# Kernel optimization log

Measured on AMD Instinct MI355X. Metric: run time of the kernel, lower is better.

Reference implementation:

```python
import jax, jax.numpy as jnp
import numpy as np

D = 512   # feature_dim
H = 256   # hidden_dim


def setup_inputs() -> dict:
    key = jax.random.key(0)
    ks = jax.random.split(key, 7)
    s = 1.0 / np.sqrt(H)
    return {
        "x": jax.random.normal(ks[0], (128, 512, D), dtype=jnp.float32),
        "W_ih": jax.random.uniform(ks[1], (4 * H, D), jnp.float32, -s, s),
        "W_hh": jax.random.uniform(ks[2], (4 * H, H), jnp.float32, -s, s),
        "b_ih": jax.random.uniform(ks[3], (4 * H,), jnp.float32, -s, s),
        "b_hh": jax.random.uniform(ks[4], (4 * H,), jnp.float32, -s, s),
        "fc_w": jax.random.uniform(ks[5], (1, H), jnp.float32, -s, s),
        "fc_b": jax.random.uniform(ks[6], (1,), jnp.float32, -s, s),
    }


def _lstm_last_hidden(x, W_ih, W_hh, b_ih, b_hh):
    # x: [B, S, D]. PyTorch gate order: i, f, g, o.
    B = x.shape[0]
    # Precompute input projections for all timesteps: [S, B, 4H]
    xg = jnp.einsum('bsd,gd->sbg', x, W_ih) + (b_ih + b_hh)

    def step(carry, xg_t):
        h, c = carry
        gates = xg_t + h @ W_hh.T  # [B, 4H]
        i, f, g, o = jnp.split(gates, 4, axis=-1)
        c = jax.nn.sigmoid(f) * c + jax.nn.sigmoid(i) * jnp.tanh(g)
        h = jax.nn.sigmoid(o) * jnp.tanh(c)
        return (h, c), None

    h0 = jnp.zeros((B, H), x.dtype)
    c0 = jnp.zeros((B, H), x.dtype)
    (h_n, _), _ = jax.lax.scan(step, (h0, c0), xg)
    return h_n  # [B, H]


def reference(x, W_ih, W_hh, b_ih, b_hh, fc_w, fc_b):
    h_n = _lstm_last_hidden(x, W_ih, W_hh, b_ih, b_hh)
    logits = h_n @ fc_w.T + fc_b  # [B, 1]
    return logits
```

## Files before the change

kernel.cpp:

```cpp
#include <hip/hip_runtime.h>
#include <stdint.h>

typedef _Float16 f16;
typedef _Float16 f16x2 __attribute__((ext_vector_type(2)));
typedef _Float16 f16x8 __attribute__((ext_vector_type(8)));
typedef float f32x4 __attribute__((ext_vector_type(4)));

#define SEQ   512
#define BATCH 128
#define DIM   512
#define HID   256
#define G4    1024

typedef const __attribute__((address_space(1))) void* gas1p;
typedef __attribute__((address_space(3))) void* las3p;

__device__ __forceinline__ uint32_t pk2(float a, float b){
  return __builtin_bit_cast(uint32_t, __builtin_amdgcn_cvt_pkrtz(a, b));
}

__device__ __forceinline__ int sdot4(uint32_t a, uint32_t b, int c){
#if __has_builtin(__builtin_amdgcn_sdot4)
  return __builtin_amdgcn_sdot4(a, b, c, false);
#else
  int s = c;
  #pragma unroll
  for (int i = 0; i < 4; ++i){
    int ai = (int)(signed char)((a >> (8*i)) & 0xff);
    int bi = (int)(signed char)((b >> (8*i)) & 0xff);
    s += ai*bi;
  }
  return s;
#endif
}

__device__ __forceinline__ float sigm(float x){
  return __builtin_amdgcn_rcpf(1.0f + __expf(-x));
}
__device__ __forceinline__ float tanh_(float x){
  return 1.0f - 2.0f*__builtin_amdgcn_rcpf(__expf(2.0f*x) + 1.0f);
}

__global__ void __launch_bounds__(256) cvt_f16_kernel(const float* __restrict__ in,
                                                      f16* __restrict__ out, int n8){
  int i = blockIdx.x*blockDim.x + threadIdx.x;
  if (i >= n8) return;
  const float4* p = (const float4*)in;
  float4 a = p[2*i], b = p[2*i+1];
  uint4 r;
  r.x = pk2(a.x, a.y); r.y = pk2(a.z, a.w);
  r.z = pk2(b.x, b.y); r.w = pk2(b.z, b.w);
  ((uint4*)out)[i] = r;
}

__global__ void __launch_bounds__(256) prep_whh8(const float* __restrict__ Whh,
                                                 uint32_t* __restrict__ W8L){
  int p = blockIdx.x*256 + threadIdx.x;
  int t  = p >> 7;
  int r  = (p >> 5) & 3;
  int qq = p & 31;
  int lane  = t & 63;
  int j     = (t >> 6)*32 + (lane & 31);
  int khalf = (lane >> 5) & 1;
  int g  = j + (r << 8);
  int kw = khalf*32 + qq;
  float4 v = *(const float4*)(Whh + g*HID + kw*4);
  int a = __float2int_rn(v.x*2048.f); a = a > 127 ? 127 : (a < -127 ? -127 : a);
  int b = __float2int_rn(v.y*2048.f); b = b > 127 ? 127 : (b < -127 ? -127 : b);
  int c = __float2int_rn(v.z*2048.f); c = c > 127 ? 127 : (c < -127 ? -127 : c);
  int d = __float2int_rn(v.w*2048.f); d = d > 127 ? 127 : (d < -127 ? -127 : d);
  W8L[p] = (uint32_t)(a & 0xff) | ((uint32_t)(b & 0xff) << 8) |
           ((uint32_t)(c & 0xff) << 16) | ((uint32_t)(d & 0xff) << 24);
}

#define BM 128
#define BN 128
#define BK 64

__global__ void __launch_bounds__(256) gemm_xg_kernel(const f16* __restrict__ A,
                                                      const f16* __restrict__ Bm,
                                                      const float* __restrict__ bih,
                                                      const float* __restrict__ bhh,
                                                      f16* __restrict__ C){
  __shared__ __align__(16) f16 ldsA[BM*BK];
  __shared__ __align__(16) f16 ldsB[BN*BK];
  const int tid  = threadIdx.x;
  const int wave = tid >> 6;
  const int lane = tid & 63;
  const int bid  = blockIdx.x;
  const int nt   = bid & 7;
  const int mt   = bid >> 3;
  const long m0  = (long)mt * BM;
  const int n0   = nt * BN;
  const int wm   = wave >> 1, wn = wave & 1;
  const int lrow = lane >> 3;
  const int lk   = (lane & 7) * 8;

  f32x4 acc[4][4];
  #pragma unroll
  for (int i=0;i<4;++i)
    #pragma unroll
    for (int j=0;j<4;++j) acc[i][j] = (f32x4){0.f,0.f,0.f,0.f};

  auto ldsAq = (__attribute__((address_space(3))) char*)ldsA;
  auto ldsBq = (__attribute__((address_space(3))) char*)ldsB;

  for (int kt = 0; kt < DIM/BK; ++kt){
    const int k0 = kt*BK;
    __syncthreads();
    #pragma unroll
    for (int i = 0; i < 4; ++i){
      const int seg = wave*4 + i;
      const f16* ga = A  + (m0 + seg*8 + lrow)*DIM + (k0 + lk);
      const f16* gb = Bm + (long)(n0 + seg*8 + lrow)*DIM + (k0 + lk);
      __builtin_amdgcn_global_load_lds((gas1p)ga, (las3p)(ldsAq + seg*1024), 16, 0, 0);
      __builtin_amdgcn_global_load_lds((gas1p)gb, (las3p)(ldsBq + seg*1024), 16, 0, 0);
    }
    __syncthreads();
    #pragma unroll
    for (int kk = 0; kk < 2; ++kk){
      f16x8 af[4], bf[4];
      const int kb = kk*32 + (lane>>4)*8;
      #pragma unroll
      for (int mi=0; mi<4; ++mi){
        af[mi] = *(const f16x8*)(ldsA + (wm*64 + mi*16 + (lane&15))*BK + kb);
        bf[mi] = *(const f16x8*)(ldsB + (wn*64 + mi*16 + (lane&15))*BK + kb);
      }
      #pragma unroll
      for (int mi=0;mi<4;++mi)
        #pragma unroll
        for (int ni=0;ni<4;++ni)
          acc[mi][ni] = __builtin_amdgcn_mfma_f32_16x16x32_f16(af[mi], bf[ni], acc[mi][ni], 0,0,0);
    }
  }
  float bias[4];
  #pragma unroll
  for (int ni=0;ni<4;++ni){
    int col = n0 + wn*64 + ni*16 + (lane&15);
    bias[ni] = bih[col] + bhh[col];
  }
  #pragma unroll
  for (int mi=0;mi<4;++mi){
    #pragma unroll
    for (int ni=0;ni<4;++ni){
      int col = n0 + wn*64 + ni*16 + (lane&15);
      int cpos = (col & 255)*4 + (col >> 8);
      #pragma unroll
      for (int r=0;r<4;++r){
        long row = m0 + wm*64 + mi*16 + (lane>>4)*4 + r;
        C[row*G4 + cpos] = (f16)(acc[mi][ni][r] + bias[ni]);
      }
    }
  }
}

__global__ void
__attribute__((amdgpu_flat_work_group_size(512, 512), amdgpu_waves_per_eu(2, 2)))
lstm8_kernel(const f16* __restrict__ xq,
             const uint32_t* __restrict__ W8L,
             const float* __restrict__ fcw,
             const float* __restrict__ fcb,
             float* __restrict__ out){
  __shared__ __align__(16) uint8_t h8[2][256];
  __shared__ float red[256];
  const int t = threadIdx.x;
  const int b = blockIdx.x;
  const int lane  = t & 63;
  const int j     = (t >> 6)*32 + (lane & 31);
  const int khalf = lane >> 5;
  const float invS = 1.0f / (2048.0f * 127.0f);

  uint32_t w[128];
  {
    const uint4* wp = (const uint4*)(W8L + (size_t)t*128);
    #pragma unroll
    for (int q8 = 0; q8 < 32; ++q8){
      uint4 u = wp[q8];
      w[4*q8+0] = u.x; w[4*q8+1] = u.y; w[4*q8+2] = u.z; w[4*q8+3] = u.w;
    }
  }
  #pragma unroll
  for (int i = 0; i < 128; ++i) asm volatile("" : "+v"(w[i]));

  if (t < 128) ((uint32_t*)h8)[t] = 0;

  const f16* xrow = xq + (long)b * SEQ * G4;
  ushort4 xv = *(const ushort4*)(xrow + j*4);
  float c = 0.f, hlast = 0.f;
  __syncthreads();

  for (int ts = 0; ts < SEQ; ++ts){
    ushort4 xc = xv;
    if (ts + 1 < SEQ) xv = *(const ushort4*)(xrow + (ts+1)*G4 + j*4);

    const uint4* hq = (const uint4*)&h8[ts & 1][khalf*128];
    uint4 hv[8];
    #pragma unroll
    for (int q = 0; q < 8; ++q) hv[q] = hq[q];

    int acc[4] = {0, 0, 0, 0};
    #pragma unroll
    for (int q = 0; q < 8; ++q){
      #pragma unroll
      for (int r = 0; r < 4; ++r){
        acc[r] = sdot4(w[r*32+4*q+0], hv[q].x, acc[r]);
        acc[r] = sdot4(w[r*32+4*q+1], hv[q].y, acc[r]);
        acc[r] = sdot4(w[r*32+4*q+2], hv[q].z, acc[r]);
        acc[r] = sdot4(w[r*32+4*q+3], hv[q].w, acc[r]);
      }
    }
    #pragma unroll
    for (int r = 0; r < 4; ++r) acc[r] += __shfl_xor(acc[r], 32);

    f16 xi  = __builtin_bit_cast(f16, xc.x), xf = __builtin_bit_cast(f16, xc.y);
    f16 xg_ = __builtin_bit_cast(f16, xc.z), xo = __builtin_bit_cast(f16, xc.w);
    float gi = (float)xi  + (float)acc[0]*invS;
    float gf = (float)xf  + (float)acc[1]*invS;
    float gg = (float)xg_ + (float)acc[2]*invS;
    float go = (float)xo  + (float)acc[3]*invS;
    float iv = sigm(gi), fv = sigm(gf), gv = tanh_(gg), ov = sigm(go);
    c     = fv*c + iv*gv;
    hlast = ov * tanh_(c);
    int hq8 = __float2int_rn(hlast * 127.f);
    if (khalf == 0) h8[(ts+1) & 1][j] = (uint8_t)(hq8 & 0xff);
    __syncthreads();
  }

  if (khalf == 0) red[j] = hlast * fcw[j];
  __syncthreads();
  if (t < 64){
    float s = red[t] + red[t+64] + red[t+128] + red[t+192];
    #pragma unroll
    for (int off = 32; off; off >>= 1) s += __shfl_down(s, off);
    if (t == 0) out[b] = s + fcb[0];
  }
}

extern "C" void kernel_launch(void* const* d_in, const int* in_sizes, int n_in,
                              void* d_out, int out_size, void* d_ws, size_t ws_size,
                              hipStream_t stream) {
  const float* x   = (const float*)d_in[0];
  const float* Wih = (const float*)d_in[1];
  const float* Whh = (const float*)d_in[2];
  const float* bih = (const float*)d_in[3];
  const float* bhh = (const float*)d_in[4];
  const float* fcw = (const float*)d_in[5];
  const float* fcb = (const float*)d_in[6];
  float* out = (float*)d_out;

  char* ws = (char*)d_ws;
  f16*      xh  = (f16*)ws;
  f16*      Wh  = (f16*)(ws + 67108864);
  f16*      xq  = (f16*)(ws + 68157440);
  uint32_t* W8L = (uint32_t*)(ws + 202375168);

  cvt_f16_kernel<<<16384, 256, 0, stream>>>(x,   xh, 33554432/8);
  cvt_f16_kernel<<<256,   256, 0, stream>>>(Wih, Wh, 524288/8);
  prep_whh8<<<256, 256, 0, stream>>>(Whh, W8L);
  gemm_xg_kernel<<<4096, 256, 0, stream>>>(xh, Wh, bih, bhh, xq);
  lstm8_kernel<<<BATCH, 512, 0, stream>>>(xq, W8L, fcw, fcb, out);
}
```

Baseline: 661.7 us.

## Use one thread per hidden unit in LSTM recurrence, o-gate weights in LDS

The recurrent kernel drops from 512 threads, with two threads per hidden unit splitting K and combining through a cross-lane shuffle, to 256 threads that each compute the full 256-long dot product for one hidden unit. The i, f and g gate weights (192 words) stay in registers, and the o-gate weights move to 64KB of dynamic LDS, read every step. The prep kernel writes the weights in these two new layouts. This removes the shuffle and halves the thread count, but doubles the serial dot-product chain per thread and adds LDS reads each timestep.

```diff
diff --git a/kernel.cpp b/kernel.cpp
--- a/kernel.cpp
+++ b/kernel.cpp
@@ -39,6 +39,11 @@
 }
 __device__ __forceinline__ float tanh_(float x){
   return 1.0f - 2.0f*__builtin_amdgcn_rcpf(__expf(2.0f*x) + 1.0f);
+}
+
+__device__ __forceinline__ int q8(float v){
+  int a = __float2int_rn(v * 2048.f);
+  return a > 127 ? 127 : (a < -127 ? -127 : a);
 }
 
 __global__ void __launch_bounds__(256) cvt_f16_kernel(const float* __restrict__ in,
@@ -54,23 +59,29 @@
 }
 
 __global__ void __launch_bounds__(256) prep_whh8(const float* __restrict__ Whh,
-                                                 uint32_t* __restrict__ W8L){
+                                                 uint32_t* __restrict__ W8R,
+                                                 uint32_t* __restrict__ W8O){
   int p = blockIdx.x*256 + threadIdx.x;
-  int t  = p >> 7;
-  int r  = (p >> 5) & 3;
-  int qq = p & 31;
-  int lane  = t & 63;
-  int j     = (t >> 6)*32 + (lane & 31);
-  int khalf = (lane >> 5) & 1;
-  int g  = j + (r << 8);
-  int kw = khalf*32 + qq;
+  int g, kw;
+  uint32_t* dst;
+  int idx;
+  if (p < 49152){
+    int t = p / 192, rem = p % 192;
+    int r = rem >> 6;
+    kw = rem & 63;
+    g = t + (r << 8);
+    dst = W8R; idx = p;
+  } else {
+    int pB = p - 49152;
+    int q4 = pB >> 10, t = (pB >> 2) & 255, w = pB & 3;
+    kw = q4*4 + w;
+    g = t + 768;
+    dst = W8O; idx = pB;
+  }
   float4 v = *(const float4*)(Whh + g*HID + kw*4);
-  int a = __float2int_rn(v.x*2048.f); a = a > 127 ? 127 : (a < -127 ? -127 : a);
-  int b = __float2int_rn(v.y*2048.f); b = b > 127 ? 127 : (b < -127 ? -127 : b);
-  int c = __float2int_rn(v.z*2048.f); c = c > 127 ? 127 : (c < -127 ? -127 : c);
-  int d = __float2int_rn(v.w*2048.f); d = d > 127 ? 127 : (d < -127 ? -127 : d);
-  W8L[p] = (uint32_t)(a & 0xff) | ((uint32_t)(b & 0xff) << 8) |
-           ((uint32_t)(c & 0xff) << 16) | ((uint32_t)(d & 0xff) << 24);
+  int a = q8(v.x), b = q8(v.y), c = q8(v.z), d = q8(v.w);
+  dst[idx] = (uint32_t)(a & 0xff) | ((uint32_t)(b & 0xff) << 8) |
+             ((uint32_t)(c & 0xff) << 16) | ((uint32_t)(d & 0xff) << 24);
 }
 
 #define BM 128
@@ -155,78 +166,73 @@
 }
 
 __global__ void
-__attribute__((amdgpu_flat_work_group_size(512, 512), amdgpu_waves_per_eu(2, 2)))
+__attribute__((amdgpu_flat_work_group_size(256, 256), amdgpu_waves_per_eu(1, 1)))
 lstm8_kernel(const f16* __restrict__ xq,
-             const uint32_t* __restrict__ W8L,
+             const uint32_t* __restrict__ W8R,
+             const uint4* __restrict__ W8O,
              const float* __restrict__ fcw,
              const float* __restrict__ fcb,
              float* __restrict__ out){
-  __shared__ __align__(16) uint8_t h8[2][256];
-  __shared__ float red[256];
+  extern __shared__ __align__(16) char smem[];
+  uint4*   WoL = (uint4*)smem;
+  uint8_t* h8  = (uint8_t*)(smem + 65536);
+  float*   red = (float*)(smem + 66048);
   const int t = threadIdx.x;
   const int b = blockIdx.x;
-  const int lane  = t & 63;
-  const int j     = (t >> 6)*32 + (lane & 31);
-  const int khalf = lane >> 5;
   const float invS = 1.0f / (2048.0f * 127.0f);
 
-  uint32_t w[128];
+  #pragma unroll
+  for (int i = 0; i < 16; ++i) WoL[i*256 + t] = W8O[i*256 + t];
+
+  uint4 w4[48];
   {
-    const uint4* wp = (const uint4*)(W8L + (size_t)t*128);
-    #pragma unroll
-    for (int q8 = 0; q8 < 32; ++q8){
-      uint4 u = wp[q8];
-      w[4*q8+0] = u.x; w[4*q8+1] = u.y; w[4*q8+2] = u.z; w[4*q8+3] = u.w;
-    }
-  }
-  #pragma unroll
-  for (int i = 0; i < 128; ++i) asm volatile("" : "+v"(w[i]));
+    const uint4* wp = (const uint4*)(W8R + (size_t)t*192);
+    #pragma unroll
+    for (int i = 0; i < 48; ++i) w4[i] = wp[i];
+  }
 
   if (t < 128) ((uint32_t*)h8)[t] = 0;
-
   const f16* xrow = xq + (long)b * SEQ * G4;
-  ushort4 xv = *(const ushort4*)(xrow + j*4);
+  ushort4 xv = *(const ushort4*)(xrow + t*4);
   float c = 0.f, hlast = 0.f;
   __syncthreads();
 
   for (int ts = 0; ts < SEQ; ++ts){
     ushort4 xc = xv;
-    if (ts + 1 < SEQ) xv = *(const ushort4*)(xrow + (ts+1)*G4 + j*4);
-
-    const uint4* hq = (const uint4*)&h8[ts & 1][khalf*128];
-    uint4 hv[8];
-    #pragma unroll
-    for (int q = 0; q < 8; ++q) hv[q] = hq[q];
-
-    int acc[4] = {0, 0, 0, 0};
-    #pragma unroll
-    for (int q = 0; q < 8; ++q){
-      #pragma unroll
-      for (int r = 0; r < 4; ++r){
-        acc[r] = sdot4(w[r*32+4*q+0], hv[q].x, acc[r]);
-        acc[r] = sdot4(w[r*32+4*q+1], hv[q].y, acc[r]);
-        acc[r] = sdot4(w[r*32+4*q+2], hv[q].z, acc[r]);
-        acc[r] = sdot4(w[r*32+4*q+3], hv[q].w, acc[r]);
-      }
-    }
-    #pragma unroll
-    for (int r = 0; r < 4; ++r) acc[r] += __shfl_xor(acc[r], 32);
+    if (ts + 1 < SEQ) xv = *(const ushort4*)(xrow + (ts+1)*G4 + t*4);
+
+    const uint4* hq = (const uint4*)&h8[(ts & 1)*256];
+    int a0 = 0, a1 = 0, a2 = 0, a3 = 0;
+    #pragma unroll
+    for (int q4 = 0; q4 < 16; ++q4){
+      uint4 hv = hq[q4];
+      uint4 wo = WoL[q4*256 + t];
+      uint4 wi = w4[q4], wf = w4[16 + q4], wg = w4[32 + q4];
+      a0 = sdot4(wi.x, hv.x, a0); a0 = sdot4(wi.y, hv.y, a0);
+      a0 = sdot4(wi.z, hv.z, a0); a0 = sdot4(wi.w, hv.w, a0);
+      a1 = sdot4(wf.x, hv.x, a1); a1 = sdot4(wf.y, hv.y, a1);
+      a1 = sdot4(wf.z, hv.z, a1); a1 = sdot4(wf.w, hv.w, a1);
+      a2 = sdot4(wg.x, hv.x, a2); a2 = sdot4(wg.y, hv.y, a2);
+      a2 = sdot4(wg.z, hv.z, a2); a2 = sdot4(wg.w, hv.w, a2);
+      a3 = sdot4(wo.x, hv.x, a3); a3 = sdot4(wo.y, hv.y, a3);
+      a3 = sdot4(wo.z, hv.z, a3); a3 = sdot4(wo.w, hv.w, a3);
+    }
 
     f16 xi  = __builtin_bit_cast(f16, xc.x), xf = __builtin_bit_cast(f16, xc.y);
     f16 xg_ = __builtin_bit_cast(f16, xc.z), xo = __builtin_bit_cast(f16, xc.w);
-    float gi = (float)xi  + (float)acc[0]*invS;
-    float gf = (float)xf  + (float)acc[1]*invS;
-    float gg = (float)xg_ + (float)acc[2]*invS;
-    float go = (float)xo  + (float)acc[3]*invS;
+    float gi = (float)xi  + (float)a0*invS;
+    float gf = (float)xf  + (float)a1*invS;
+    float gg = (float)xg_ + (float)a2*invS;
+    float go = (float)xo  + (float)a3*invS;
     float iv = sigm(gi), fv = sigm(gf), gv = tanh_(gg), ov = sigm(go);
     c     = fv*c + iv*gv;
     hlast = ov * tanh_(c);
-    int hq8 = __float2int_rn(hlast * 127.f);
-    if (khalf == 0) h8[(ts+1) & 1][j] = (uint8_t)(hq8 & 0xff);
+    int hv8 = __float2int_rn(hlast * 127.f);
+    h8[((ts+1) & 1)*256 + t] = (uint8_t)(hv8 & 0xff);
     __syncthreads();
   }
 
-  if (khalf == 0) red[j] = hlast * fcw[j];
+  red[t] = hlast * fcw[t];
   __syncthreads();
   if (t < 64){
     float s = red[t] + red[t+64] + red[t+128] + red[t+192];
@@ -252,11 +258,15 @@
   f16*      xh  = (f16*)ws;
   f16*      Wh  = (f16*)(ws + 67108864);
   f16*      xq  = (f16*)(ws + 68157440);
-  uint32_t* W8L = (uint32_t*)(ws + 202375168);
+  uint32_t* W8R = (uint32_t*)(ws + 202375168);
+  uint32_t* W8O = (uint32_t*)(ws + 202571776);
 
   cvt_f16_kernel<<<16384, 256, 0, stream>>>(x,   xh, 33554432/8);
   cvt_f16_kernel<<<256,   256, 0, stream>>>(Wih, Wh, 524288/8);
-  prep_whh8<<<256, 256, 0, stream>>>(Whh, W8L);
+  prep_whh8<<<256, 256, 0, stream>>>(Whh, W8R, W8O);
   gemm_xg_kernel<<<4096, 256, 0, stream>>>(xh, Wh, bih, bhh, xq);
-  lstm8_kernel<<<BATCH, 512, 0, stream>>>(xq, W8L, fcw, fcb, out);
-}
+  (void)hipFuncSetAttribute(reinterpret_cast<const void*>(lstm8_kernel),
+                            hipFuncAttributeMaxDynamicSharedMemorySize, 67072);
+  lstm8_kernel<<<BATCH, 256, 67072, stream>>>(xq, W8R, (const uint4*)W8O,
+                                              fcw, fcb, out);
+}
```

After: 671.5 us. No clear change (+1.5%).

## Split int8 W_hh across LDS, global/L2 and registers in LSTM recurrence

Applied to the files above, without the earlier changes.

The W_hh int8 weights are no longer held entirely in 128 VGPRs per thread. They are split three ways: 6 of 16 column chunks live in LDS (96KB of dynamic shared memory), 6 are streamed from global memory through L2 each step, and 4 stay in registers. The work is also remapped so each thread computes two gates over the full K dimension instead of four gates over half of K. This removes the per-gate cross-half shuffle and replaces it with a single shuffle that exchanges i*g. The intent is to free registers and raise occupancy or ILP, at the cost of LDS and L2 traffic on every serial timestep.

```diff
diff --git a/kernel.cpp b/kernel.cpp
--- a/kernel.cpp
+++ b/kernel.cpp
@@ -34,11 +34,28 @@
 #endif
 }
 
+__device__ __forceinline__ int dotq(uint4 w, uint4 h, int acc){
+  acc = sdot4(w.x, h.x, acc);
+  acc = sdot4(w.y, h.y, acc);
+  acc = sdot4(w.z, h.z, acc);
+  acc = sdot4(w.w, h.w, acc);
+  return acc;
+}
+
 __device__ __forceinline__ float sigm(float x){
   return __builtin_amdgcn_rcpf(1.0f + __expf(-x));
 }
 __device__ __forceinline__ float tanh_(float x){
   return 1.0f - 2.0f*__builtin_amdgcn_rcpf(__expf(2.0f*x) + 1.0f);
+}
+
+__device__ __forceinline__ uint32_t q8pack(float4 v){
+  int a = __float2int_rn(v.x*2048.f); a = a > 127 ? 127 : (a < -127 ? -127 : a);
+  int b = __float2int_rn(v.y*2048.f); b = b > 127 ? 127 : (b < -127 ? -127 : b);
+  int c = __float2int_rn(v.z*2048.f); c = c > 127 ? 127 : (c < -127 ? -127 : c);
+  int d = __float2int_rn(v.w*2048.f); d = d > 127 ? 127 : (d < -127 ? -127 : d);
+  return (uint32_t)(a & 0xff) | ((uint32_t)(b & 0xff) << 8) |
+         ((uint32_t)(c & 0xff) << 16) | ((uint32_t)(d & 0xff) << 24);
 }
 
 __global__ void __launch_bounds__(256) cvt_f16_kernel(const float* __restrict__ in,
@@ -54,23 +71,35 @@
 }
 
 __global__ void __launch_bounds__(256) prep_whh8(const float* __restrict__ Whh,
-                                                 uint32_t* __restrict__ W8L){
-  int p = blockIdx.x*256 + threadIdx.x;
-  int t  = p >> 7;
-  int r  = (p >> 5) & 3;
-  int qq = p & 31;
-  int lane  = t & 63;
-  int j     = (t >> 6)*32 + (lane & 31);
-  int khalf = (lane >> 5) & 1;
-  int g  = j + (r << 8);
-  int kw = khalf*32 + qq;
-  float4 v = *(const float4*)(Whh + g*HID + kw*4);
-  int a = __float2int_rn(v.x*2048.f); a = a > 127 ? 127 : (a < -127 ? -127 : a);
-  int b = __float2int_rn(v.y*2048.f); b = b > 127 ? 127 : (b < -127 ? -127 : b);
-  int c = __float2int_rn(v.z*2048.f); c = c > 127 ? 127 : (c < -127 ? -127 : c);
-  int d = __float2int_rn(v.w*2048.f); d = d > 127 ? 127 : (d < -127 ? -127 : d);
-  W8L[p] = (uint32_t)(a & 0xff) | ((uint32_t)(b & 0xff) << 8) |
-           ((uint32_t)(c & 0xff) << 16) | ((uint32_t)(d & 0xff) << 24);
+                                                 uint4* __restrict__ WL,
+                                                 uint4* __restrict__ WG,
+                                                 uint4* __restrict__ WR){
+  int tid = blockIdx.x*256 + threadIdx.x;
+  int r, Q; uint4* dst; int idx;
+  if (tid < 6144){
+    const int QLt[6] = {0,1,2,8,9,10};
+    int q = tid >> 10; r = tid & 1023;
+    Q = QLt[q]; dst = WL; idx = tid;
+  } else if (tid < 12288){
+    const int QGt[6] = {3,4,5,11,12,13};
+    int i = tid - 6144;
+    int q = i >> 10; r = i & 1023;
+    Q = QGt[q]; dst = WG; idx = i;
+  } else {
+    const int QRt[4] = {6,7,14,15};
+    int i = tid - 12288;
+    int t = i >> 3, s = i & 7;
+    int lane = t & 63, wave = t >> 6;
+    int j = wave*32 + (lane & 31), p = lane >> 5;
+    r = (s < 4) ? (j + p*256) : (j + p*256 + 512);
+    Q = QRt[s & 3]; dst = WR; idx = i;
+  }
+  const float* src = Whh + r*HID + Q*16;
+  float4 v0 = *(const float4*)(src);
+  float4 v1 = *(const float4*)(src + 4);
+  float4 v2 = *(const float4*)(src + 8);
+  float4 v3 = *(const float4*)(src + 12);
+  dst[idx] = make_uint4(q8pack(v0), q8pack(v1), q8pack(v2), q8pack(v3));
 }
 
 #define BM 128
@@ -155,78 +184,118 @@
 }
 
 __global__ void
-__attribute__((amdgpu_flat_work_group_size(512, 512), amdgpu_waves_per_eu(2, 2)))
+__attribute__((amdgpu_flat_work_group_size(512, 512)))
 lstm8_kernel(const f16* __restrict__ xq,
-             const uint32_t* __restrict__ W8L,
+             const uint4* __restrict__ WLg,
+             const uint4* __restrict__ WG,
+             const uint4* __restrict__ WR,
              const float* __restrict__ fcw,
              const float* __restrict__ fcb,
              float* __restrict__ out){
-  __shared__ __align__(16) uint8_t h8[2][256];
-  __shared__ float red[256];
+  extern __shared__ __align__(16) char smem[];
+  uint4*   WL  = (uint4*)smem;
+  uint8_t* h8  = (uint8_t*)(smem + 98304);
+  float*   red = (float*)(smem + 98816);
   const int t = threadIdx.x;
   const int b = blockIdx.x;
-  const int lane  = t & 63;
-  const int j     = (t >> 6)*32 + (lane & 31);
-  const int khalf = lane >> 5;
+  const int lane = t & 63, wave = t >> 6;
+  const int j = wave*32 + (lane & 31);
+  const int p = lane >> 5;
   const float invS = 1.0f / (2048.0f * 127.0f);
 
-  uint32_t w[128];
+  #pragma unroll
+  for (int i = 0; i < 12; ++i) WL[i*512 + t] = WLg[i*512 + t];
+
+  uint4 wr[8];
   {
-    const uint4* wp = (const uint4*)(W8L + (size_t)t*128);
-    #pragma unroll
-    for (int q8 = 0; q8 < 32; ++q8){
-      uint4 u = wp[q8];
-      w[4*q8+0] = u.x; w[4*q8+1] = u.y; w[4*q8+2] = u.z; w[4*q8+3] = u.w;
-    }
-  }
-  #pragma unroll
-  for (int i = 0; i < 128; ++i) asm volatile("" : "+v"(w[i]));
+    const uint4* wp = WR + (size_t)t*8;
+    #pragma unroll
+    for (int i = 0; i < 8; ++i) wr[i] = wp[i];
+  }
 
   if (t < 128) ((uint32_t*)h8)[t] = 0;
 
   const f16* xrow = xq + (long)b * SEQ * G4;
   ushort4 xv = *(const ushort4*)(xrow + j*4);
   float c = 0.f, hlast = 0.f;
+  const int r0 = j + p*256;
+  const int r1 = r0 + 512;
+  uintptr_t wga = (uintptr_t)WG;
   __syncthreads();
 
   for (int ts = 0; ts < SEQ; ++ts){
     ushort4 xc = xv;
     if (ts + 1 < SEQ) xv = *(const ushort4*)(xrow + (ts+1)*G4 + j*4);
 
-    const uint4* hq = (const uint4*)&h8[ts & 1][khalf*128];
-    uint4 hv[8];
-    #pragma unroll
-    for (int q = 0; q < 8; ++q) hv[q] = hq[q];
-
-    int acc[4] = {0, 0, 0, 0};
-    #pragma unroll
-    for (int q = 0; q < 8; ++q){
-      #pragma unroll
-      for (int r = 0; r < 4; ++r){
-        acc[r] = sdot4(w[r*32+4*q+0], hv[q].x, acc[r]);
-        acc[r] = sdot4(w[r*32+4*q+1], hv[q].y, acc[r]);
-        acc[r] = sdot4(w[r*32+4*q+2], hv[q].z, acc[r]);
-        acc[r] = sdot4(w[r*32+4*q+3], hv[q].w, acc[r]);
-      }
-    }
-    #pragma unroll
-    for (int r = 0; r < 4; ++r) acc[r] += __shfl_xor(acc[r], 32);
-
-    f16 xi  = __builtin_bit_cast(f16, xc.x), xf = __builtin_bit_cast(f16, xc.y);
-    f16 xg_ = __builtin_bit_cast(f16, xc.z), xo = __builtin_bit_cast(f16, xc.w);
-    float gi = (float)xi  + (float)acc[0]*invS;
-    float gf = (float)xf  + (float)acc[1]*invS;
-    float gg = (float)xg_ + (float)acc[2]*invS;
-    float go = (float)xo  + (float)acc[3]*invS;
-    float iv = sigm(gi), fv = sigm(gf), gv = tanh_(gg), ov = sigm(go);
-    c     = fv*c + iv*gv;
-    hlast = ov * tanh_(c);
-    int hq8 = __float2int_rn(hlast * 127.f);
-    if (khalf == 0) h8[(ts+1) & 1][j] = (uint8_t)(hq8 & 0xff);
+    uint32_t wlo = 0;
+    asm("" : "+v"(wlo));
+    asm("" : "+v"(wga));
+    const uint4* wgp = (const uint4*)wga;
+    const uint4* hq = (const uint4*)&h8[(ts & 1)*256];
+
+    int a0 = 0, a1 = 0;
+    {
+      uint4 hv[8];
+      #pragma unroll
+      for (int q = 0; q < 8; ++q) hv[q] = hq[q];
+      #pragma unroll
+      for (int q = 0; q < 3; ++q){
+        uint4 w0 = WL[wlo + q*1024 + r0];
+        uint4 w1 = WL[wlo + q*1024 + r1];
+        a0 = dotq(w0, hv[q], a0);
+        a1 = dotq(w1, hv[q], a1);
+      }
+      #pragma unroll
+      for (int q = 0; q < 3; ++q){
+        uint4 w0 = wgp[q*1024 + r0];
+        uint4 w1 = wgp[q*1024 + r1];
+        a0 = dotq(w0, hv[3+q], a0);
+        a1 = dotq(w1, hv[3+q], a1);
+      }
+      a0 = dotq(wr[0], hv[6], a0);
+      a0 = dotq(wr[1], hv[7], a0);
+      a1 = dotq(wr[4], hv[6], a1);
+      a1 = dotq(wr[5], hv[7], a1);
+    }
+    {
+      uint4 hv[8];
+      #pragma unroll
+      for (int q = 0; q < 8; ++q) hv[q] = hq[8 + q];
+      #pragma unroll
+      for (int q = 0; q < 3; ++q){
+        uint4 w0 = WL[wlo + (3+q)*1024 + r0];
+        uint4 w1 = WL[wlo + (3+q)*1024 + r1];
+        a0 = dotq(w0, hv[q], a0);
+        a1 = dotq(w1, hv[q], a1);
+      }
+      #pragma unroll
+      for (int q = 0; q < 3; ++q){
+        uint4 w0 = wgp[(3+q)*1024 + r0];
+        uint4 w1 = wgp[(3+q)*1024 + r1];
+        a0 = dotq(w0, hv[3+q], a0);
+        a1 = dotq(w1, hv[3+q], a1);
+      }
+      a0 = dotq(wr[2], hv[6], a0);
+      a0 = dotq(wr[3], hv[7], a0);
+      a1 = dotq(wr[6], hv[6], a1);
+      a1 = dotq(wr[7], hv[7], a1);
+    }
+
+    ushort xlo = p ? xc.y : xc.x;
+    ushort xhi = p ? xc.w : xc.z;
+    float gA = (float)__builtin_bit_cast(f16, xlo) + (float)a0*invS;
+    float gB = (float)__builtin_bit_cast(f16, xhi) + (float)a1*invS;
+    float IG  = sigm(gA) * tanh_(gB);
+    float IGx = __shfl_xor(IG, 32);
+    if (p){
+      c     = sigm(gA)*c + IGx;
+      hlast = sigm(gB) * tanh_(c);
+      h8[((ts+1) & 1)*256 + j] = (uint8_t)(__float2int_rn(hlast*127.f) & 0xff);
+    }
     __syncthreads();
   }
 
-  if (khalf == 0) red[j] = hlast * fcw[j];
+  if (p) red[j] = hlast * fcw[j];
   __syncthreads();
   if (t < 64){
     float s = red[t] + red[t+64] + red[t+128] + red[t+192];
@@ -249,14 +318,18 @@
   float* out = (float*)d_out;
 
   char* ws = (char*)d_ws;
-  f16*      xh  = (f16*)ws;
-  f16*      Wh  = (f16*)(ws + 67108864);
-  f16*      xq  = (f16*)(ws + 68157440);
-  uint32_t* W8L = (uint32_t*)(ws + 202375168);
+  f16*   xh  = (f16*)ws;
+  f16*   Wh  = (f16*)(ws + 67108864);
+  f16*   xq  = (f16*)(ws + 68157440);
+  uint4* WL  = (uint4*)(ws + 202375168);
+  uint4* WG  = (uint4*)(ws + 202473472);
+  uint4* WR  = (uint4*)(ws + 202571776);
 
   cvt_f16_kernel<<<16384, 256, 0, stream>>>(x,   xh, 33554432/8);
   cvt_f16_kernel<<<256,   256, 0, stream>>>(Wih, Wh, 524288/8);
-  prep_whh8<<<256, 256, 0, stream>>>(Whh, W8L);
+  prep_whh8<<<64, 256, 0, stream>>>(Whh, WL, WG, WR);
   gemm_xg_kernel<<<4096, 256, 0, stream>>>(xh, Wh, bih, bhh, xq);
-  lstm8_kernel<<<BATCH, 512, 0, stream>>>(xq, W8L, fcw, fcb, out);
-}
+  (void)hipFuncSetAttribute(reinterpret_cast<const void*>(lstm8_kernel),
+                            hipFuncAttributeMaxDynamicSharedMemorySize, 99840);
+  lstm8_kernel<<<BATCH, 512, 99840, stream>>>(xq, WL, WG, WR, fcw, fcb, out);
+}
```

After: 1.064 ms. 60.7% more time.

## Split recurrent int8 weights across registers, LDS and global memory

Applied to the files above, without the earlier changes.

The recurrent int8 weight slice per thread (128 dwords) no longer sits entirely in VGPRs. A quarter stays in registers, a quarter is staged into 64KB of dynamic LDS, and half is re-read from global memory (L1/L2) every timestep. The prep kernel writes three separate layouts to match. This lowers register pressure and drops the waves_per_eu constraint, but adds LDS and global loads on the serial per-step critical path.

```diff
diff --git a/kernel.cpp b/kernel.cpp
--- a/kernel.cpp
+++ b/kernel.cpp
@@ -2,7 +2,6 @@
 #include <stdint.h>
 
 typedef _Float16 f16;
-typedef _Float16 f16x2 __attribute__((ext_vector_type(2)));
 typedef _Float16 f16x8 __attribute__((ext_vector_type(8)));
 typedef float f32x4 __attribute__((ext_vector_type(4)));
 
@@ -34,11 +33,27 @@
 #endif
 }
 
+__device__ __forceinline__ int dotq(uint4 w, uint4 h, int acc){
+  acc = sdot4(w.x, h.x, acc);
+  acc = sdot4(w.y, h.y, acc);
+  acc = sdot4(w.z, h.z, acc);
+  acc = sdot4(w.w, h.w, acc);
+  return acc;
+}
+
 __device__ __forceinline__ float sigm(float x){
   return __builtin_amdgcn_rcpf(1.0f + __expf(-x));
 }
 __device__ __forceinline__ float tanh_(float x){
   return 1.0f - 2.0f*__builtin_amdgcn_rcpf(__expf(2.0f*x) + 1.0f);
+}
+__device__ __forceinline__ uint32_t q8pack(float4 v){
+  int a = __float2int_rn(v.x*2048.f); a = a > 127 ? 127 : (a < -127 ? -127 : a);
+  int b = __float2int_rn(v.y*2048.f); b = b > 127 ? 127 : (b < -127 ? -127 : b);
+  int c = __float2int_rn(v.z*2048.f); c = c > 127 ? 127 : (c < -127 ? -127 : c);
+  int d = __float2int_rn(v.w*2048.f); d = d > 127 ? 127 : (d < -127 ? -127 : d);
+  return (uint32_t)(a & 0xff) | ((uint32_t)(b & 0xff) << 8) |
+         ((uint32_t)(c & 0xff) << 16) | ((uint32_t)(d & 0xff) << 24);
 }
 
 __global__ void __launch_bounds__(256) cvt_f16_kernel(const float* __restrict__ in,
@@ -54,23 +69,27 @@
 }
 
 __global__ void __launch_bounds__(256) prep_whh8(const float* __restrict__ Whh,
-                                                 uint32_t* __restrict__ W8L){
-  int p = blockIdx.x*256 + threadIdx.x;
-  int t  = p >> 7;
-  int r  = (p >> 5) & 3;
-  int qq = p & 31;
+                                                 uint4* __restrict__ WR,
+                                                 uint4* __restrict__ WLg,
+                                                 uint4* __restrict__ WG){
+  int tid = blockIdx.x*256 + threadIdx.x;
+  int t  = tid & 511;
+  int qi = tid >> 9;
+  int r  = qi >> 3, Q = qi & 7;
   int lane  = t & 63;
   int j     = (t >> 6)*32 + (lane & 31);
-  int khalf = (lane >> 5) & 1;
+  int khalf = lane >> 5;
   int g  = j + (r << 8);
-  int kw = khalf*32 + qq;
-  float4 v = *(const float4*)(Whh + g*HID + kw*4);
-  int a = __float2int_rn(v.x*2048.f); a = a > 127 ? 127 : (a < -127 ? -127 : a);
-  int b = __float2int_rn(v.y*2048.f); b = b > 127 ? 127 : (b < -127 ? -127 : b);
-  int c = __float2int_rn(v.z*2048.f); c = c > 127 ? 127 : (c < -127 ? -127 : c);
-  int d = __float2int_rn(v.w*2048.f); d = d > 127 ? 127 : (d < -127 ? -127 : d);
-  W8L[p] = (uint32_t)(a & 0xff) | ((uint32_t)(b & 0xff) << 8) |
-           ((uint32_t)(c & 0xff) << 16) | ((uint32_t)(d & 0xff) << 24);
+  int kw = khalf*32 + Q*4;
+  const float* src = Whh + g*HID + kw*4;
+  float4 v0 = *(const float4*)(src);
+  float4 v1 = *(const float4*)(src + 4);
+  float4 v2 = *(const float4*)(src + 8);
+  float4 v3 = *(const float4*)(src + 12);
+  uint4 pk = make_uint4(q8pack(v0), q8pack(v1), q8pack(v2), q8pack(v3));
+  if (Q < 2)      WR [(r*2 + Q    )*512 + t] = pk;
+  else if (Q < 4) WLg[(r*2 + Q - 2)*512 + t] = pk;
+  else            WG [(r*4 + Q - 4)*512 + t] = pk;
 }
 
 #define BM 128
@@ -155,14 +174,18 @@
 }
 
 __global__ void
-__attribute__((amdgpu_flat_work_group_size(512, 512), amdgpu_waves_per_eu(2, 2)))
+__attribute__((amdgpu_flat_work_group_size(512, 512)))
 lstm8_kernel(const f16* __restrict__ xq,
-             const uint32_t* __restrict__ W8L,
+             const uint4* __restrict__ WR,
+             const uint4* __restrict__ WLg,
+             const uint4* __restrict__ WG,
              const float* __restrict__ fcw,
              const float* __restrict__ fcb,
              float* __restrict__ out){
-  __shared__ __align__(16) uint8_t h8[2][256];
-  __shared__ float red[256];
+  extern __shared__ __align__(16) char smem[];
+  uint4*   WL  = (uint4*)smem;
+  uint8_t* h8  = (uint8_t*)(smem + 65536);
+  float*   red = (float*)(smem + 66048);
   const int t = threadIdx.x;
   const int b = blockIdx.x;
   const int lane  = t & 63;
@@ -170,44 +193,48 @@
   const int khalf = lane >> 5;
   const float invS = 1.0f / (2048.0f * 127.0f);
 
-  uint32_t w[128];
+  #pragma unroll
+  for (int i = 0; i < 8; ++i) WL[i*512 + t] = WLg[i*512 + t];
+
+  uint4 wr[8];
   {
-    const uint4* wp = (const uint4*)(W8L + (size_t)t*128);
-    #pragma unroll
-    for (int q8 = 0; q8 < 32; ++q8){
-      uint4 u = wp[q8];
-      w[4*q8+0] = u.x; w[4*q8+1] = u.y; w[4*q8+2] = u.z; w[4*q8+3] = u.w;
-    }
-  }
-  #pragma unroll
-  for (int i = 0; i < 128; ++i) asm volatile("" : "+v"(w[i]));
+    #pragma unroll
+    for (int i = 0; i < 8; ++i) wr[i] = WR[i*512 + t];
+  }
 
   if (t < 128) ((uint32_t*)h8)[t] = 0;
 
   const f16* xrow = xq + (long)b * SEQ * G4;
   ushort4 xv = *(const ushort4*)(xrow + j*4);
   float c = 0.f, hlast = 0.f;
+  uintptr_t wga = (uintptr_t)WG;
   __syncthreads();
 
   for (int ts = 0; ts < SEQ; ++ts){
     ushort4 xc = xv;
     if (ts + 1 < SEQ) xv = *(const ushort4*)(xrow + (ts+1)*G4 + j*4);
 
-    const uint4* hq = (const uint4*)&h8[ts & 1][khalf*128];
+    uint32_t wlo = 0;
+    asm("" : "+v"(wlo));
+    asm("" : "+v"(wga));
+    const uint4* wgp = (const uint4*)wga;
+    const uint4* hq = (const uint4*)&h8[(ts & 1)*256 + khalf*128];
     uint4 hv[8];
     #pragma unroll
     for (int q = 0; q < 8; ++q) hv[q] = hq[q];
 
-    int acc[4] = {0, 0, 0, 0};
-    #pragma unroll
-    for (int q = 0; q < 8; ++q){
-      #pragma unroll
-      for (int r = 0; r < 4; ++r){
-        acc[r] = sdot4(w[r*32+4*q+0], hv[q].x, acc[r]);
-        acc[r] = sdot4(w[r*32+4*q+1], hv[q].y, acc[r]);
-        acc[r] = sdot4(w[r*32+4*q+2], hv[q].z, acc[r]);
-        acc[r] = sdot4(w[r*32+4*q+3], hv[q].w, acc[r]);
-      }
+    int acc[4];
+    #pragma unroll
+    for (int r = 0; r < 4; ++r){
+      int a = 0;
+      a = dotq(wr[r*2 + 0], hv[0], a);
+      a = dotq(wr[r*2 + 1], hv[1], a);
+      a = dotq(WL[wlo + (r*2+0)*512 + t], hv[2], a);
+      a = dotq(WL[wlo + (r*2+1)*512 + t], hv[3], a);
+      #pragma unroll
+      for (int qg = 0; qg < 4; ++qg)
+        a = dotq(wgp[(r*4+qg)*512 + t], hv[4+qg], a);
+      acc[r] = a;
     }
     #pragma unroll
     for (int r = 0; r < 4; ++r) acc[r] += __shfl_xor(acc[r], 32);
@@ -222,7 +249,7 @@
     c     = fv*c + iv*gv;
     hlast = ov * tanh_(c);
     int hq8 = __float2int_rn(hlast * 127.f);
-    if (khalf == 0) h8[(ts+1) & 1][j] = (uint8_t)(hq8 & 0xff);
+    if (khalf == 0) h8[((ts+1) & 1)*256 + j] = (uint8_t)(hq8 & 0xff);
     __syncthreads();
   }
 
@@ -249,14 +276,18 @@
   float* out = (float*)d_out;
 
   char* ws = (char*)d_ws;
-  f16*      xh  = (f16*)ws;
-  f16*      Wh  = (f16*)(ws + 67108864);
-  f16*      xq  = (f16*)(ws + 68157440);
-  uint32_t* W8L = (uint32_t*)(ws + 202375168);
+  f16*   xh  = (f16*)ws;
+  f16*   Wh  = (f16*)(ws + 67108864);
+  f16*   xq  = (f16*)(ws + 68157440);
+  uint4* WR  = (uint4*)(ws + 202375168);
+  uint4* WLg = (uint4*)(ws + 202440704);
+  uint4* WG  = (uint4*)(ws + 202506240);
 
   cvt_f16_kernel<<<16384, 256, 0, stream>>>(x,   xh, 33554432/8);
   cvt_f16_kernel<<<256,   256, 0, stream>>>(Wih, Wh, 524288/8);
-  prep_whh8<<<256, 256, 0, stream>>>(Whh, W8L);
+  prep_whh8<<<64, 256, 0, stream>>>(Whh, WR, WLg, WG);
   gemm_xg_kernel<<<4096, 256, 0, stream>>>(xh, Wh, bih, bhh, xq);
-  lstm8_kernel<<<BATCH, 512, 0, stream>>>(xq, W8L, fcw, fcb, out);
-}
+  (void)hipFuncSetAttribute(reinterpret_cast<const void*>(lstm8_kernel),
+                            hipFuncAttributeMaxDynamicSharedMemorySize, 67072);
+  lstm8_kernel<<<BATCH, 512, 67072, stream>>>(xq, WR, WLg, WG, fcw, fcb, out);
+}
```

New measurement: 1.063 ms. 1.61x slower.
